# Kernel optimization log

Hardware: AMD Instinct MI355X
Metric: run time of the kernel (lower is better)

## Reference

```python
import jax, jax.numpy as jnp
import numpy as np

DIM = 1024
NUM_HEADS = 16
HEAD_DIM = 64  # DIM // NUM_HEADS
BATCH = 2
SEQ = 2048


def setup_inputs() -> dict:
    key = jax.random.key(0)
    ks = jax.random.split(key, 6)
    x = jax.random.normal(ks[0], (BATCH, SEQ, DIM), dtype=jnp.float32)
    # Linear weights stored as [in, out] so y = x @ W (same math as torch Linear).
    Wq = jax.random.normal(ks[1], (DIM, DIM), dtype=jnp.float32) * (DIM ** -0.5)
    # MQA: single shared KV head of size HEAD_DIM.
    Wk = jax.random.normal(ks[2], (DIM, HEAD_DIM), dtype=jnp.float32) * (DIM ** -0.5)
    Wv = jax.random.normal(ks[3], (DIM, HEAD_DIM), dtype=jnp.float32) * (DIM ** -0.5)
    Wo = jax.random.normal(ks[4], (DIM, DIM), dtype=jnp.float32) * (DIM ** -0.5)
    bo = jax.random.normal(ks[5], (DIM,), dtype=jnp.float32) * 0.01
    return {"x": x, "Wq": Wq, "Wk": Wk, "Wv": Wv, "Wo": Wo, "bo": bo}


def reference(x, Wq, Wk, Wv, Wo, bo):
    b, s, _ = x.shape
    scale = HEAD_DIM ** -0.5
    # Per-head queries [b, h, s, d]
    q = (x @ Wq).reshape(b, s, NUM_HEADS, HEAD_DIM).transpose(0, 2, 1, 3) * scale
    # Shared single KV head [b, s, d]
    k = x @ Wk
    v = x @ Wv
    # Materialized scores [b, h, s_q, s_k]
    scores = jnp.einsum('bhqd,bkd->bhqk', q, k)
    causal = jnp.tril(jnp.ones((s, s), dtype=bool))  # True where allowed
    scores = jnp.where(causal, scores, -jnp.inf)
    # Manual stable softmax (max, exp, sum, div) as in the original
    max_scores = jnp.max(scores, axis=-1, keepdims=True)
    exp_scores = jnp.exp(scores - max_scores)
    attn = exp_scores / jnp.sum(exp_scores, axis=-1, keepdims=True)
    out = jnp.einsum('bhqk,bkd->bhqd', attn, v)  # [b, h, s, d]
    out = out.transpose(0, 2, 1, 3).reshape(b, s, DIM)
    return out @ Wo + bo
```

## Files before the change

### kernel.cpp

```cpp
#include <hip/hip_runtime.h>

typedef unsigned short u16;
typedef __attribute__((ext_vector_type(8))) short short8;
typedef __attribute__((ext_vector_type(4))) float f32x4;

static __device__ __forceinline__ u16 f32_to_bf16(float f) {
  unsigned u = __float_as_uint(f);
  u += 0x7fffu + ((u >> 16) & 1u);
  return (u16)(u >> 16);
}

static __device__ __forceinline__ unsigned cvt_pk_bf16(float a, float b) {
  unsigned r;
  asm("v_cvt_pk_bf16_f32 %0, %1, %2" : "=v"(r) : "v"(a), "v"(b));
  return r;
}

static __device__ __forceinline__ void async16(u16* lds, const u16* g) {
  __builtin_amdgcn_global_load_lds(
      (const __attribute__((address_space(1))) void*)g,
      (__attribute__((address_space(3))) void*)lds, 16, 0, 0);
}


__global__ void __launch_bounds__(256) prep_kernel(
    const float* __restrict__ x,
    const float* __restrict__ Wq, const float* __restrict__ Wk,
    const float* __restrict__ Wv, const float* __restrict__ Wo,
    u16* __restrict__ Xb, u16* __restrict__ WqT, u16* __restrict__ WkvT,
    u16* __restrict__ WoT) {
  __shared__ u16 T[64][72];
  int id = blockIdx.x;
  int tid = threadIdx.x;
  if (id < 2048) {
    int base = (id * 256 + tid) * 8;
    float4 a = *(const float4*)&x[base];
    float4 b = *(const float4*)&x[base + 4];
    short8 v;
    v[0] = (short)f32_to_bf16(a.x); v[1] = (short)f32_to_bf16(a.y);
    v[2] = (short)f32_to_bf16(a.z); v[3] = (short)f32_to_bf16(a.w);
    v[4] = (short)f32_to_bf16(b.x); v[5] = (short)f32_to_bf16(b.y);
    v[6] = (short)f32_to_bf16(b.z); v[7] = (short)f32_to_bf16(b.w);
    *(short8*)&Xb[base] = v;
    return;
  }
  int id2 = id - 2048;
  const float* src; u16* dst; int tk, tn, src_ld, row_off;
  if (id2 < 256)      { src = Wq; dst = WqT;  tk = id2 & 15; tn = id2 >> 4; src_ld = 1024; row_off = 0; }
  else if (id2 < 512) { int i = id2 - 256; src = Wo; dst = WoT; tk = i & 15; tn = i >> 4; src_ld = 1024; row_off = 0; }
  else if (id2 < 528) { src = Wk; dst = WkvT; tk = id2 - 512; tn = 0; src_ld = 64; row_off = 0; }
  else                { src = Wv; dst = WkvT; tk = id2 - 528; tn = 0; src_ld = 64; row_off = 64; }
  int k0 = tk * 64, n0 = tn * 64;
#pragma unroll
  for (int it = 0; it < 2; ++it) {
    int c = tid + it * 256;
    int r = c >> 3, cc = (c & 7) * 8;
    const float* p = &src[(k0 + r) * src_ld + n0 + cc];
    float4 a = *(const float4*)&p[0];
    float4 b = *(const float4*)&p[4];
    short8 v;
    v[0] = (short)f32_to_bf16(a.x); v[1] = (short)f32_to_bf16(a.y);
    v[2] = (short)f32_to_bf16(a.z); v[3] = (short)f32_to_bf16(a.w);
    v[4] = (short)f32_to_bf16(b.x); v[5] = (short)f32_to_bf16(b.y);
    v[6] = (short)f32_to_bf16(b.z); v[7] = (short)f32_to_bf16(b.w);
    *(short8*)&T[r][cc] = v;
  }
  __syncthreads();
#pragma unroll
  for (int it = 0; it < 2; ++it) {
    int c = tid + it * 256;
    int r = c >> 3, cc = (c & 7) * 8;
    short8 v;
#pragma unroll
    for (int j = 0; j < 8; ++j) v[j] = (short)T[cc + j][r];
    *(short8*)&dst[(row_off + n0 + r) * 1024 + k0 + cc] = v;
  }
}

__device__ __forceinline__ void stage_64x128(
    const u16* __restrict__ A, const u16* __restrict__ BT, int m0, int K,
    int k0, u16* As, u16* Bs, int w, int lrow, int swz8) {
#pragma unroll
  for (int it = 0; it < 2; ++it) {
    int W = w * 2 + it;
    async16(As + W * 512, &A[(size_t)(m0 + W * 8 + lrow) * K + k0 + swz8]);
  }
#pragma unroll
  for (int it = 0; it < 4; ++it) {
    int W = w * 4 + it;
    async16(Bs + W * 512, &BT[(size_t)(W * 8 + lrow) * K + k0 + swz8]);
  }
}

__device__ __forceinline__ void gemm_core_64x128_db(
    const u16* __restrict__ A, const u16* __restrict__ BT, int m0, int K,
    f32x4 (&acc)[2][4], u16* As, u16* Bs,
    int lane, int w, int wr, int wc, int g, int lo) {
  int lrow = lane >> 3;
  int swz8 = ((lane & 7) ^ lrow) * 8;
  int lo7 = lo & 7;
  const int NK = K >> 6;
  stage_64x128(A, BT, m0, K, 0, As, Bs, w, lrow, swz8);
  for (int kt = 0; kt < NK; ++kt) {
    int cur = kt & 1;
    __syncthreads();
    if (kt + 1 < NK)
      stage_64x128(A, BT, m0, K, (kt + 1) * 64,
                   As + (cur ^ 1) * 4096, Bs + (cur ^ 1) * 8192, w, lrow, swz8);
    const u16* Asc = As + cur * 4096;
    const u16* Bsc = Bs + cur * 8192;
#pragma unroll
    for (int ks = 0; ks < 2; ++ks) {
      int pc = ((ks * 4 + g) ^ lo7) * 8;
      short8 af[2], bf[4];
#pragma unroll
      for (int i = 0; i < 2; ++i)
        af[i] = *(const short8*)&Asc[(wr * 32 + i * 16 + lo) * 64 + pc];
#pragma unroll
      for (int i = 0; i < 4; ++i)
        bf[i] = *(const short8*)&Bsc[(wc * 64 + i * 16 + lo) * 64 + pc];
#pragma unroll
      for (int mi = 0; mi < 2; ++mi)
#pragma unroll
        for (int ni = 0; ni < 4; ++ni)
          acc[mi][ni] = __builtin_amdgcn_mfma_f32_16x16x32_bf16(
              af[mi], bf[ni], acc[mi][ni], 0, 0, 0);
    }
  }
}

__global__ void __launch_bounds__(256) qkv_gemm(
    const u16* __restrict__ Xb, const u16* __restrict__ WqT,
    const u16* __restrict__ WkvT, u16* __restrict__ Qb, u16* __restrict__ KVb,
    u16* __restrict__ VTb) {
  __shared__ u16 As[2 * 64 * 64];
  __shared__ u16 Bs[2 * 128 * 64];
  int tid = threadIdx.x, lane = tid & 63, w = tid >> 6;
  int wr = w >> 1, wc = w & 1, g = lane >> 4, lo = lane & 15;
  int m0 = blockIdx.x * 64, nb = blockIdx.y;
  const u16* BT = (nb < 8) ? (WqT + (size_t)nb * 128 * 1024) : WkvT;
  f32x4 acc[2][4];
  f32x4 zz = {0.f, 0.f, 0.f, 0.f};
#pragma unroll
  for (int i = 0; i < 2; ++i)
#pragma unroll
    for (int j = 0; j < 4; ++j) acc[i][j] = zz;
  gemm_core_64x128_db(Xb, BT, m0, 1024, acc, As, Bs, lane, w, wr, wc, g, lo);
#pragma unroll
  for (int mi = 0; mi < 2; ++mi)
#pragma unroll
    for (int ni = 0; ni < 4; ++ni)
#pragma unroll
      for (int r = 0; r < 4; ++r) {
        int row = m0 + wr * 32 + mi * 16 + g * 4 + r;
        int col = wc * 64 + ni * 16 + lo;
        u16 v = f32_to_bf16(acc[mi][ni][r]);
        if (nb < 8) {
          Qb[row * 1024 + nb * 128 + col] = v;
        } else if (wc == 0) {
          KVb[row * 64 + col] = v;
        } else {
          int d = col - 64;
          VTb[(((row >> 11) * 64) + d) * 2048 + (row & 2047)] = v;
        }
      }
}

__global__ void __launch_bounds__(256, 2) attn_kernel(
    const u16* __restrict__ Qb, const u16* __restrict__ KVb,
    const u16* __restrict__ VTb, u16* __restrict__ AOb) {
  __shared__ u16 Ks[2][128 * 64];
  __shared__ u16 Vt[2][2][64 * 64];
  __shared__ u16 Ps[4][2][16][64];
  int tid = threadIdx.x, lane = tid & 63, w = tid >> 6;
  int gq = lane >> 4, lo = lane & 15;
  int hg = blockIdx.y;
  int b = blockIdx.z;
  int a = b ? (31 - (int)blockIdx.x) : (int)blockIdx.x;
  int qb = a * 64 + w * 16;
  int lrow = lane >> 3;
  int swz8 = ((lane & 7) ^ lrow) * 8;
  int lo7 = lo & 7;

  short8 qf[2][2];
#pragma unroll
  for (int h = 0; h < 2; ++h) {
    const u16* qp = &Qb[(size_t)(b * 2048 + qb + lo) * 1024 + (hg * 2 + h) * 64];
    qf[h][0] = *(const short8*)&qp[gq * 8];
    qf[h][1] = *(const short8*)&qp[32 + gq * 8];
  }

  f32x4 zz = {0.f, 0.f, 0.f, 0.f};
  f32x4 oacc[2][4];
  float lsum[2] = {0.f, 0.f};
#pragma unroll
  for (int h = 0; h < 2; ++h)
#pragma unroll
    for (int i = 0; i < 4; ++i) oacc[h][i] = zz;

  const float kExp = 0.18033688011112042f;
  const float kOff = 11.541560327111707f;

  auto stage_kv = [&](int t, int bu) {
#pragma unroll
    for (int it = 0; it < 4; ++it) {
      int seg = w * 4 + it;
      async16(&Ks[bu][seg * 512],
              &KVb[(size_t)(b * 2048 + t * 128 + seg * 8 + lrow) * 64 + swz8]);
      int kk = seg >> 3, s2 = seg & 7;
      async16(&Vt[bu][kk][s2 * 512],
              &VTb[((size_t)b * 64 + s2 * 8 + lrow) * 2048 + t * 128 + kk * 64 + swz8]);
    }
  };

  int nst = (a >> 1) + 1;
  stage_kv(0, 0);
  for (int t = 0; t < nst; ++t) {
    int cur = t & 1;
    __syncthreads();
    if (t + 1 < nst) stage_kv(t + 1, cur ^ 1);
#pragma unroll
    for (int kk = 0; kk < 2; ++kk) {
      int kt = 2 * t + kk;
      if (kt <= a) {
        const u16* Kck = &Ks[cur][kk * 4096];
        const u16* Vc = Vt[cur][kk];

        f32x4 sacc[2][4];
#pragma unroll
        for (int h = 0; h < 2; ++h)
#pragma unroll
          for (int ns = 0; ns < 4; ++ns) sacc[h][ns] = zz;
#pragma unroll
        for (int ks = 0; ks < 2; ++ks) {
          int pc = ((ks * 4 + gq) ^ lo7) * 8;
          short8 kf[4];
#pragma unroll
          for (int ns = 0; ns < 4; ++ns)
            kf[ns] = *(const short8*)&Kck[(ns * 16 + lo) * 64 + pc];
#pragma unroll
          for (int ns = 0; ns < 4; ++ns)
#pragma unroll
            for (int h = 0; h < 2; ++h)
              sacc[h][ns] = __builtin_amdgcn_mfma_f32_16x16x32_bf16(
                  kf[ns], qf[h][ks], sacc[h][ns], 0, 0, 0);
        }

        bool diag = (kt == a);
        int qg = qb + lo;
#pragma unroll
        for (int h = 0; h < 2; ++h)
#pragma unroll
          for (int ns = 0; ns < 4; ++ns) {
            float p[4];
#pragma unroll
            for (int r = 0; r < 4; ++r) {
              float pv = __builtin_amdgcn_exp2f(fmaf(sacc[h][ns][r], kExp, -kOff));
              if (diag) {
                int kg = kt * 64 + ns * 16 + gq * 4 + r;
                if (kg > qg) pv = 0.f;
              }
              lsum[h] += pv;
              p[r] = pv;
            }
            uint2 pd;
            pd.x = cvt_pk_bf16(p[0], p[1]);
            pd.y = cvt_pk_bf16(p[2], p[3]);
            int ch = (2 * ns + (gq >> 1)) ^ lo7;
            *(uint2*)&Ps[w][h][lo][ch * 8 + (gq & 1) * 4] = pd;
          }
        __threadfence_block();

#pragma unroll
        for (int k2 = 0; k2 < 2; ++k2) {
          int pc = ((k2 * 4 + gq) ^ lo7) * 8;
          short8 vf[4];
#pragma unroll
          for (int ds = 0; ds < 4; ++ds)
            vf[ds] = *(const short8*)&Vc[(ds * 16 + lo) * 64 + pc];
          short8 pf[2];
#pragma unroll
          for (int h = 0; h < 2; ++h)
            pf[h] = *(const short8*)&Ps[w][h][lo][pc];
#pragma unroll
          for (int h = 0; h < 2; ++h)
#pragma unroll
            for (int ds = 0; ds < 4; ++ds)
              oacc[h][ds] = __builtin_amdgcn_mfma_f32_16x16x32_bf16(
                  vf[ds], pf[h], oacc[h][ds], 0, 0, 0);
        }
      }
    }
  }

  int row = b * 2048 + qb + lo;
#pragma unroll
  for (int h = 0; h < 2; ++h) {
    float ls = lsum[h];
    ls += __shfl_xor(ls, 16);
    ls += __shfl_xor(ls, 32);
    float inv = 1.0f / ls;
#pragma unroll
    for (int ds = 0; ds < 4; ++ds) {
      uint2 od;
      od.x = cvt_pk_bf16(oacc[h][ds][0] * inv, oacc[h][ds][1] * inv);
      od.y = cvt_pk_bf16(oacc[h][ds][2] * inv, oacc[h][ds][3] * inv);
      *(uint2*)&AOb[(size_t)row * 1024 + (hg * 2 + h) * 64 + ds * 16 + gq * 4] = od;
    }
  }
}

__global__ void __launch_bounds__(256) out_gemm(
    const u16* __restrict__ A, const u16* __restrict__ WoT,
    const float* __restrict__ bias, float* __restrict__ C) {
  __shared__ u16 As[2 * 64 * 64];
  __shared__ u16 Bs[2 * 128 * 64];
  int tid = threadIdx.x, lane = tid & 63, w = tid >> 6;
  int wr = w >> 1, wc = w & 1, g = lane >> 4, lo = lane & 15;
  int m0 = blockIdx.x * 64, nb = blockIdx.y;
  const u16* BT = WoT + (size_t)nb * 128 * 1024;
  f32x4 acc[2][4];
  f32x4 zz = {0.f, 0.f, 0.f, 0.f};
#pragma unroll
  for (int i = 0; i < 2; ++i)
#pragma unroll
    for (int j = 0; j < 4; ++j) acc[i][j] = zz;
  gemm_core_64x128_db(A, BT, m0, 1024, acc, As, Bs, lane, w, wr, wc, g, lo);
#pragma unroll
  for (int mi = 0; mi < 2; ++mi)
#pragma unroll
    for (int ni = 0; ni < 4; ++ni)
#pragma unroll
      for (int r = 0; r < 4; ++r) {
        int row = m0 + wr * 32 + mi * 16 + g * 4 + r;
        int col = nb * 128 + wc * 64 + ni * 16 + lo;
        C[row * 1024 + col] = acc[mi][ni][r] + bias[col];
      }
}

extern "C" void kernel_launch(void* const* d_in, const int* in_sizes, int n_in,
                              void* d_out, int out_size, void* d_ws, size_t ws_size,
                              hipStream_t stream) {
  const float* x  = (const float*)d_in[0];
  const float* Wq = (const float*)d_in[1];
  const float* Wk = (const float*)d_in[2];
  const float* Wv = (const float*)d_in[3];
  const float* Wo = (const float*)d_in[4];
  const float* bo = (const float*)d_in[5];
  float* out = (float*)d_out;

  u16* ws   = (u16*)d_ws;
  u16* AOb  = ws;
  u16* KVb  = AOb + 4194304;
  u16* VTb  = KVb + 262144;
  u16* Xb   = VTb + 262144;
  u16* WqT  = Xb + 4194304;
  u16* WoT  = WqT + 1048576;
  u16* WkvT = WoT + 1048576;
  u16* Qb   = (u16*)d_out;

  prep_kernel<<<2592, 256, 0, stream>>>(x, Wq, Wk, Wv, Wo, Xb, WqT, WkvT, WoT);
  qkv_gemm<<<dim3(64, 9), 256, 0, stream>>>(Xb, WqT, WkvT, Qb, KVb, VTb);
  attn_kernel<<<dim3(32, 8, 2), 256, 0, stream>>>(Qb, KVb, VTb, AOb);
  out_gemm<<<dim3(64, 8), 256, 0, stream>>>(AOb, WoT, bo, out);
}
```

Baseline: 159.3 us.

## Keep P in registers and use 16x16x16 MFMA for PV, dropping LDS round-trip

The softmax probabilities now stay in registers and feed the PV product directly. The PV product switches from 16x16x32 to 16x16x16 bf16 MFMA, whose K layout matches the score accumulator layout. This removes the per-warp LDS P buffer, its stores and reloads, and the block fence. In exchange it issues twice as many smaller MFMAs with narrower V loads, and adds s_setprio hints around the MFMA bursts.

```diff
diff --git a/kernel.cpp b/kernel.cpp
--- a/kernel.cpp
+++ b/kernel.cpp
@@ -2,6 +2,7 @@
 
 typedef unsigned short u16;
 typedef __attribute__((ext_vector_type(8))) short short8;
+typedef __attribute__((ext_vector_type(4))) short s16x4;
 typedef __attribute__((ext_vector_type(4))) float f32x4;
 
 static __device__ __forceinline__ u16 f32_to_bf16(float f) {
@@ -14,6 +15,15 @@
   unsigned r;
   asm("v_cvt_pk_bf16_f32 %0, %1, %2" : "=v"(r) : "v"(a), "v"(b));
   return r;
+}
+
+static __device__ __forceinline__ f32x4 mfma16(s16x4 a, s16x4 b, f32x4 c) {
+#if defined(__HIP_DEVICE_COMPILE__)
+  return __builtin_amdgcn_mfma_f32_16x16x16bf16_1k(a, b, c, 0, 0, 0);
+#else
+  (void)a; (void)b;
+  return c;
+#endif
 }
 
 static __device__ __forceinline__ void async16(u16* lds, const u16* g) {
@@ -171,7 +181,6 @@
     const u16* __restrict__ VTb, u16* __restrict__ AOb) {
   __shared__ u16 Ks[2][128 * 64];
   __shared__ u16 Vt[2][2][64 * 64];
-  __shared__ u16 Ps[4][2][16][64];
   int tid = threadIdx.x, lane = tid & 63, w = tid >> 6;
   int gq = lane >> 4, lo = lane & 15;
   int hg = blockIdx.y;
@@ -238,16 +247,19 @@
 #pragma unroll
           for (int ns = 0; ns < 4; ++ns)
             kf[ns] = *(const short8*)&Kck[(ns * 16 + lo) * 64 + pc];
+          __builtin_amdgcn_s_setprio(1);
 #pragma unroll
           for (int ns = 0; ns < 4; ++ns)
 #pragma unroll
             for (int h = 0; h < 2; ++h)
               sacc[h][ns] = __builtin_amdgcn_mfma_f32_16x16x32_bf16(
                   kf[ns], qf[h][ks], sacc[h][ns], 0, 0, 0);
+          __builtin_amdgcn_s_setprio(0);
         }
 
         bool diag = (kt == a);
         int qg = qb + lo;
+        uint2 pfu[2][4];
 #pragma unroll
         for (int h = 0; h < 2; ++h)
 #pragma unroll
@@ -263,31 +275,25 @@
               lsum[h] += pv;
               p[r] = pv;
             }
-            uint2 pd;
-            pd.x = cvt_pk_bf16(p[0], p[1]);
-            pd.y = cvt_pk_bf16(p[2], p[3]);
-            int ch = (2 * ns + (gq >> 1)) ^ lo7;
-            *(uint2*)&Ps[w][h][lo][ch * 8 + (gq & 1) * 4] = pd;
+            pfu[h][ns].x = cvt_pk_bf16(p[0], p[1]);
+            pfu[h][ns].y = cvt_pk_bf16(p[2], p[3]);
           }
-        __threadfence_block();
-
-#pragma unroll
-        for (int k2 = 0; k2 < 2; ++k2) {
-          int pc = ((k2 * 4 + gq) ^ lo7) * 8;
-          short8 vf[4];
+
+#pragma unroll
+        for (int ns = 0; ns < 4; ++ns) {
+          int co = ((2 * ns + (gq >> 1)) ^ lo7) * 8 + (gq & 1) * 4;
+          s16x4 vf[4];
 #pragma unroll
           for (int ds = 0; ds < 4; ++ds)
-            vf[ds] = *(const short8*)&Vc[(ds * 16 + lo) * 64 + pc];
-          short8 pf[2];
-#pragma unroll
-          for (int h = 0; h < 2; ++h)
-            pf[h] = *(const short8*)&Ps[w][h][lo][pc];
-#pragma unroll
-          for (int h = 0; h < 2; ++h)
-#pragma unroll
-            for (int ds = 0; ds < 4; ++ds)
-              oacc[h][ds] = __builtin_amdgcn_mfma_f32_16x16x32_bf16(
-                  vf[ds], pf[h], oacc[h][ds], 0, 0, 0);
+            vf[ds] = *(const s16x4*)&Vc[(ds * 16 + lo) * 64 + co];
+          __builtin_amdgcn_s_setprio(1);
+#pragma unroll
+          for (int ds = 0; ds < 4; ++ds)
+#pragma unroll
+            for (int h = 0; h < 2; ++h)
+              oacc[h][ds] = mfma16(vf[ds], *(const s16x4*)&pfu[h][ns],
+                                   oacc[h][ds]);
+          __builtin_amdgcn_s_setprio(0);
         }
       }
     }
```

New measurement: 161.9 us. No clear change (+1.7%).
